# Kernel tuning notes

Hardware: AMD Instinct MI355X
Metric: run time of the kernel (lower is better)

Reference implementation:

```python
import jax, jax.numpy as jnp
import numpy as np

N, E = 50000, 800000          # nodes, edges
F_IN, H, C = 32, 64, 7        # input feats, hidden, classes
EPS = 1e-5                    # BatchNorm eps


def setup_inputs() -> dict:
    key = jax.random.key(0)
    ks = jax.random.split(key, 16)
    inp = {
        "x": jax.random.normal(ks[0], (N, F_IN), jnp.float32),
        "edge_index": jax.random.randint(ks[1], (2, E), 0, N),
        "edge_attr": jax.random.uniform(ks[2], (E, 1), jnp.float32),
    }

    def conv_params(k, cin, cout, i):
        k1, k2 = jax.random.split(k)
        s = 1.0 / np.sqrt(cin)
        inp[f"W{i}"] = jax.random.uniform(k1, (2, cin, cout), jnp.float32, -s, s)  # spline kernel weights
        inp[f"R{i}"] = jax.random.uniform(k2, (cin, cout), jnp.float32, -s, s)     # root weight
        inp[f"B{i}"] = jnp.zeros((cout,), jnp.float32)

    conv_params(ks[3], F_IN, H, 0)
    conv_params(ks[4], H, H, 1)
    conv_params(ks[5], H, C, 2)
    for i in range(2):  # BatchNorm (eval mode: running stats)
        inp[f"G{i}"] = jnp.ones((H,), jnp.float32)
        inp[f"BE{i}"] = jnp.zeros((H,), jnp.float32)
        inp[f"RM{i}"] = 0.1 * jax.random.normal(ks[6 + 2 * i], (H,), jnp.float32)
        inp[f"RV{i}"] = jax.random.uniform(ks[7 + 2 * i], (H,), jnp.float32, 0.5, 1.5)
    return inp


def spline_conv(x, src, dst, u, W, R, B):
    # dim=1, kernel_size=2, degree=1 open B-spline:
    # basis = (1-u, u) with weight indices (0, 1) for u in [0,1).
    basis = jnp.stack([1.0 - u, u], axis=1)               # [E, 2]
    msg = jnp.einsum('ec,ek,kco->eo', x[src], basis, W)    # gather + basis-weighted linear
    agg = jax.ops.segment_sum(msg, dst, num_segments=N)    # scatter-add
    deg = jax.ops.segment_sum(jnp.ones((src.shape[0],), x.dtype), dst, num_segments=N)
    agg = agg / jnp.maximum(deg, 1.0)[:, None]             # aggr='mean' (default)
    return agg + x @ R + B                                 # root weight + bias


def batch_norm(x, g, b, rm, rv):
    return (x - rm) * jax.lax.rsqrt(rv + EPS) * g + b


def reference(x, edge_index, edge_attr,
              W0, R0, B0, W1, R1, B1, W2, R2, B2,
              G0, BE0, RM0, RV0, G1, BE1, RM1, RV1):
    src, dst = edge_index[0], edge_index[1]
    u = edge_attr[:, 0]
    h = spline_conv(x, src, dst, u, W0, R0, B0)
    h = jax.nn.elu(batch_norm(h, G0, BE0, RM0, RV0))
    h = spline_conv(h, src, dst, u, W1, R1, B1)
    h = jax.nn.elu(batch_norm(h, G1, BE1, RM1, RV1))
    h = spline_conv(h, src, dst, u, W2, R2, B2)
    return jax.nn.log_softmax(h, axis=1)
```

## Files before the change

### kernel.cpp

```cpp
#include <hip/hip_runtime.h>
#include <hip/hip_fp16.h>
#include <math.h>

#define NN 50000
#define NE 800000
#define EPSV 1e-5f
#define BSHIFT 7
#define BSIZE 128
#define NB 391
#define CAP 2560

typedef _Float16 h2f   __attribute__((ext_vector_type(2)));
typedef _Float16 f16x8 __attribute__((ext_vector_type(8)));
typedef float    f32x4 __attribute__((ext_vector_type(4)));

__global__ __launch_bounds__(64) void prep_all_kernel(
        const float* __restrict__ W0, const float* __restrict__ R0,
        const float* __restrict__ W1, const float* __restrict__ R1,
        const float* __restrict__ W2, const float* __restrict__ R2,
        __half* __restrict__ Bf0, __half* __restrict__ Bf1, __half* __restrict__ Bf7,
        int* __restrict__ bcursor) {
    int lane = threadIdx.x;
    int bid = blockIdx.x;
    int c = lane & 15;
    int kbase = ((lane >> 4) << 3);
    _Float16 vals[8];
    if (bid < 12) {
        int nt = bid;
        int n = nt * 16 + c;
#pragma unroll
        for (int j = 0; j < 8; ++j) {
            int k = kbase + j;
            float v;
            if (n < 64)       v = W0[k * 64 + n];
            else if (n < 128) v = W0[32 * 64 + k * 64 + (n - 64)];
            else              v = R0[k * 64 + (n - 128)];
            vals[j] = (_Float16)v;
        }
        *reinterpret_cast<f16x8*>(Bf0 + ((size_t)(bid * 64 + lane)) * 8) =
            *reinterpret_cast<f16x8*>(vals);
    } else if (bid < 36) {
        int ksnt = bid - 12;
        int ks = ksnt / 12, nt = ksnt - ks * 12;
        int n = nt * 16 + c;
#pragma unroll
        for (int j = 0; j < 8; ++j) {
            int k = ks * 32 + kbase + j;
            float v;
            if (n < 64)       v = W1[k * 64 + n];
            else if (n < 128) v = W1[64 * 64 + k * 64 + (n - 64)];
            else              v = R1[k * 64 + (n - 128)];
            vals[j] = (_Float16)v;
        }
        *reinterpret_cast<f16x8*>(Bf1 + ((size_t)(ksnt * 64 + lane)) * 8) =
            *reinterpret_cast<f16x8*>(vals);
    } else if (bid < 40) {
        int ksnt = bid - 36;
        int ks = ksnt >> 1, nt = ksnt & 1;
#pragma unroll
        for (int j = 0; j < 8; ++j) {
            int k = ks * 32 + kbase + j;
            float v = 0.f;
            if (nt == 0) {
                if (c < 7)                 v = W2[k * 7 + c];
                else if (c >= 8 && c < 15) v = W2[448 + k * 7 + (c - 8)];
            } else {
                if (c < 7)                 v = R2[k * 7 + c];
            }
            vals[j] = (_Float16)v;
        }
        *reinterpret_cast<f16x8*>(Bf7 + ((size_t)(ksnt * 64 + lane)) * 8) =
            *reinterpret_cast<f16x8*>(vals);
    } else {
        int b = (bid - 40) * 64 + lane;
        if (b < NB) bcursor[b] = b * CAP;
    }
}

template<int CIN, bool AHALF>
__device__ __forceinline__ void gemm_body(int bx, int tid,
                               const void* __restrict__ xin,
                               const __half* __restrict__ Bfrag,
                               const float* __restrict__ Bb,
                               __half2* __restrict__ YabH,
                               float* __restrict__ Z,
                               int n_nodes) {
    const int lane = tid & 63;
    const int wid  = tid >> 6;
    int m0 = (bx * 4 + wid) * 16;
    if (m0 >= n_nodes) return;
    const int KS = CIN / 32;

    f32x4 acc[12];
#pragma unroll
    for (int i = 0; i < 12; ++i) acc[i] = (f32x4){0.f, 0.f, 0.f, 0.f};

    const int arow = m0 + (lane & 15);
    const int koff = ((lane >> 4) << 3);
    const f16x8* bf = reinterpret_cast<const f16x8*>(Bfrag);
#pragma unroll
    for (int ks = 0; ks < KS; ++ks) {
        f16x8 av;
        if constexpr (AHALF) {
            const _Float16* ap = (const _Float16*)xin + (size_t)arow * CIN + ks * 32 + koff;
            av = *reinterpret_cast<const f16x8*>(ap);
        } else {
            const float* ap = (const float*)xin + (size_t)arow * CIN + ks * 32 + koff;
            float4 a0 = *reinterpret_cast<const float4*>(ap);
            float4 a1 = *reinterpret_cast<const float4*>(ap + 4);
            av[0] = (_Float16)a0.x; av[1] = (_Float16)a0.y;
            av[2] = (_Float16)a0.z; av[3] = (_Float16)a0.w;
            av[4] = (_Float16)a1.x; av[5] = (_Float16)a1.y;
            av[6] = (_Float16)a1.z; av[7] = (_Float16)a1.w;
        }
#pragma unroll
        for (int nt = 0; nt < 12; ++nt) {
            f16x8 bv = bf[(ks * 12 + nt) * 64 + lane];
            acc[nt] = __builtin_amdgcn_mfma_f32_16x16x32_f16(av, bv, acc[nt], 0, 0, 0);
        }
    }

    const int c_lo  = lane & 15;
    const int rbase = ((lane >> 4) << 2);
#pragma unroll
    for (int r = 0; r < 4; ++r) {
        int row = m0 + rbase + r;
#pragma unroll
        for (int nt = 0; nt < 4; ++nt) {
            int c = nt * 16 + c_lo;
            YabH[(size_t)row * 64 + c] = __floats2half2_rn(acc[nt][r], acc[nt + 4][r]);
        }
#pragma unroll
        for (int nt = 8; nt < 12; ++nt) {
            int c = (nt - 8) * 16 + c_lo;
            Z[(size_t)row * 64 + c] = acc[nt][r] + Bb[c];
        }
    }
}

__global__ __launch_bounds__(256) void binB_gemm0_kernel(
        const int* __restrict__ src, const int* __restrict__ dst,
        const float* __restrict__ attr, int* __restrict__ bcursor,
        unsigned* __restrict__ es1su, unsigned char* __restrict__ es1dl, int E,
        const float* __restrict__ x, const __half* __restrict__ Bf0,
        const float* __restrict__ Bb0, __half2* __restrict__ YabH,
        float* __restrict__ Z, int n_nodes) {
    __shared__ int hist[NB];
    __shared__ int base[NB];
    if (blockIdx.x >= NB) {
        gemm_body<32, false>(blockIdx.x - NB, threadIdx.x, x, Bf0, Bb0, YabH, Z, n_nodes);
        return;
    }
    for (int i = threadIdx.x; i < NB; i += blockDim.x) hist[i] = 0;
    __syncthreads();
    const int chunk = (E + NB - 1) / NB;
    int e0 = blockIdx.x * chunk;
    int e1 = e0 + chunk; if (e1 > E) e1 = E;
    unsigned su[8]; unsigned char dlv[8]; short bv[8];
#pragma unroll
    for (int j = 0; j < 8; ++j) {
        int e = e0 + threadIdx.x + j * 256;
        if (e < e1) {
            int d = dst[e];
            int b = d >> BSHIFT;
            __half uh = __float2half_rn(attr[e]);
            su[j]  = ((unsigned)src[e] << 16) | (unsigned)__half_as_ushort(uh);
            dlv[j] = (unsigned char)(d & (BSIZE - 1));
            bv[j]  = (short)b;
            atomicAdd(&hist[b], 1);
        }
    }
    __syncthreads();
    for (int i = threadIdx.x; i < NB; i += blockDim.x) {
        int c = hist[i];
        base[i] = c ? atomicAdd(&bcursor[i], c) : 0;
        hist[i] = 0;
    }
    __syncthreads();
#pragma unroll
    for (int j = 0; j < 8; ++j) {
        int e = e0 + threadIdx.x + j * 256;
        if (e < e1) {
            int b = bv[j];
            int slot = base[b] + atomicAdd(&hist[b], 1);
            es1su[slot] = su[j];
            es1dl[slot] = dlv[j];
        }
    }
}

__global__ __launch_bounds__(256) void gemm1_kernel(const __half* __restrict__ h,
                               const __half* __restrict__ Bf1,
                               const float* __restrict__ Bb,
                               __half2* __restrict__ YabH,
                               float* __restrict__ Z, int n_nodes) {
    gemm_body<64, true>(blockIdx.x, threadIdx.x, h, Bf1, Bb, YabH, Z, n_nodes);
}

__global__ __launch_bounds__(256) void placeC_kernel(const int* __restrict__ bcursor,
                                                     const unsigned* __restrict__ es1su,
                                                     const unsigned char* __restrict__ es1dl,
                                                     int2* __restrict__ rowrange,
                                                     uint2* __restrict__ es8) {
    __shared__ int hist[BSIZE];
    __shared__ int stmp[BSIZE];
    __shared__ int cur[BSIZE];
    int b = blockIdx.x;
    int t = threadIdx.x;
    int bs = b * CAP;
    int be = bcursor[b];
    if (t < BSIZE) hist[t] = 0;
    __syncthreads();
    unsigned su[10]; unsigned char dlv[10];
#pragma unroll
    for (int j = 0; j < 10; ++j) {
        int i = bs + t + j * 256;
        if (i < be) {
            su[j]  = es1su[i];
            dlv[j] = es1dl[i];
            atomicAdd(&hist[dlv[j]], 1);
        }
    }
    __syncthreads();
    if (t < BSIZE) {
        int v = hist[t];
        int incl = v;
#pragma unroll
        for (int o = 1; o < 64; o <<= 1) {
            int nv = __shfl_up(incl, o, 64);
            if ((t & 63) >= o) incl += nv;
        }
        stmp[t] = incl;
    }
    __syncthreads();
    if (t < BSIZE) {
        int excl = stmp[t] - hist[t] + ((t >= 64) ? stmp[63] : 0);
        cur[t] = excl;
        int node = b * BSIZE + t;
        if (node < NN) {
            int2 rr; rr.x = bs + excl; rr.y = bs + excl + hist[t];
            rowrange[node] = rr;
        }
    }
    __syncthreads();
#pragma unroll
    for (int j = 0; j < 10; ++j) {
        int i = bs + t + j * 256;
        if (i < be) {
            unsigned r = su[j];
            int dl = dlv[j];
            int slot = bs + atomicAdd(&cur[dl], 1);
            __half uh = __ushort_as_half((unsigned short)(r & 0xffffu));
            __half2 p = __halves2half2(__hsub(__ushort_as_half((unsigned short)0x3C00u), uh), uh);
            uint2 rec;
            rec.x = r >> 16;
            rec.y = *reinterpret_cast<unsigned*>(&p);
            es8[slot] = rec;
        }
    }
}

__global__ __launch_bounds__(256) void gemm7_kernel(const __half* __restrict__ h,
                               const __half* __restrict__ Bf7,
                               const float* __restrict__ Bb,
                               __half* __restrict__ Yab7H,
                               float* __restrict__ Z7,
                               int n_nodes) {
    const int lane = threadIdx.x & 63;
    const int wid  = threadIdx.x >> 6;
    int m0 = (blockIdx.x * 4 + wid) * 16;
    if (m0 >= n_nodes) return;

    f32x4 acc[2];
    acc[0] = (f32x4){0.f, 0.f, 0.f, 0.f};
    acc[1] = (f32x4){0.f, 0.f, 0.f, 0.f};
    const int arow = m0 + (lane & 15);
    const int koff = ((lane >> 4) << 3);
    const f16x8* bf = reinterpret_cast<const f16x8*>(Bf7);
#pragma unroll
    for (int ks = 0; ks < 2; ++ks) {
        f16x8 av = *reinterpret_cast<const f16x8*>(
            (const _Float16*)h + (size_t)arow * 64 + ks * 32 + koff);
#pragma unroll
        for (int nt = 0; nt < 2; ++nt) {
            f16x8 bv = bf[(ks * 2 + nt) * 64 + lane];
            acc[nt] = __builtin_amdgcn_mfma_f32_16x16x32_f16(av, bv, acc[nt], 0, 0, 0);
        }
    }
    const int c_lo  = lane & 15;
    const int rbase = ((lane >> 4) << 2);
#pragma unroll
    for (int r = 0; r < 4; ++r) {
        int row = m0 + rbase + r;
        if (c_lo < 7) {
            Yab7H[(size_t)row * 14 + 2 * c_lo] = __float2half(acc[0][r]);
            Z7[(size_t)row * 7 + c_lo] = acc[1][r] + Bb[c_lo];
        } else if (c_lo >= 8 && c_lo < 15) {
            Yab7H[(size_t)row * 14 + 2 * (c_lo - 8) + 1] = __float2half(acc[0][r]);
        }
    }
}

__global__ void gather64_kernel(const int2* __restrict__ rowrange,
                                const uint2* __restrict__ es8,
                                const __half2* __restrict__ YabH,
                                const float* __restrict__ Z,
                                const float* __restrict__ G, const float* __restrict__ BE,
                                const float* __restrict__ RM, const float* __restrict__ RV,
                                __half* __restrict__ h, int n_nodes) {
    int n = (blockIdx.x * blockDim.x + threadIdx.x) >> 6;
    int lane = threadIdx.x & 63;
    if (n >= n_nodes) return;
    int2 rr = rowrange[n];
    int beg = __builtin_amdgcn_readfirstlane(rr.x);
    int end = __builtin_amdgcn_readfirstlane(rr.y);
    const char* Ybase = (const char*)YabH + 4 * lane;
    float acc0 = 0.f, acc1 = 0.f, acc2 = 0.f, acc3 = 0.f;
    float acc4 = 0.f, acc5 = 0.f, acc6 = 0.f, acc7 = 0.f;
    int i = beg;
    if (i < end && (i & 1)) {
        uint2 q = es8[i];
        __half2 v = *(const __half2*)(Ybase + ((size_t)q.x << 8));
        acc0 = __builtin_amdgcn_fdot2(__builtin_bit_cast(h2f, v), __builtin_bit_cast(h2f, q.y), acc0, false);
        ++i;
    }
    for (; i + 15 < end; i += 16) {
        uint4 q0 = *reinterpret_cast<const uint4*>(es8 + i);
        uint4 q1 = *reinterpret_cast<const uint4*>(es8 + i + 2);
        uint4 q2 = *reinterpret_cast<const uint4*>(es8 + i + 4);
        uint4 q3 = *reinterpret_cast<const uint4*>(es8 + i + 6);
        uint4 q4 = *reinterpret_cast<const uint4*>(es8 + i + 8);
        uint4 q5 = *reinterpret_cast<const uint4*>(es8 + i + 10);
        uint4 q6 = *reinterpret_cast<const uint4*>(es8 + i + 12);
        uint4 q7 = *reinterpret_cast<const uint4*>(es8 + i + 14);
        __half2 v0 = *(const __half2*)(Ybase + ((size_t)q0.x << 8));
        __half2 v1 = *(const __half2*)(Ybase + ((size_t)q0.z << 8));
        __half2 v2 = *(const __half2*)(Ybase + ((size_t)q1.x << 8));
        __half2 v3 = *(const __half2*)(Ybase + ((size_t)q1.z << 8));
        __half2 v4 = *(const __half2*)(Ybase + ((size_t)q2.x << 8));
        __half2 v5 = *(const __half2*)(Ybase + ((size_t)q2.z << 8));
        __half2 v6 = *(const __half2*)(Ybase + ((size_t)q3.x << 8));
        __half2 v7 = *(const __half2*)(Ybase + ((size_t)q3.z << 8));
        __half2 v8 = *(const __half2*)(Ybase + ((size_t)q4.x << 8));
        __half2 v9 = *(const __half2*)(Ybase + ((size_t)q4.z << 8));
        __half2 va = *(const __half2*)(Ybase + ((size_t)q5.x << 8));
        __half2 vb = *(const __half2*)(Ybase + ((size_t)q5.z << 8));
        __half2 vc = *(const __half2*)(Ybase + ((size_t)q6.x << 8));
        __half2 vd = *(const __half2*)(Ybase + ((size_t)q6.z << 8));
        __half2 ve = *(const __half2*)(Ybase + ((size_t)q7.x << 8));
        __half2 vf = *(const __half2*)(Ybase + ((size_t)q7.z << 8));
        acc0 = __builtin_amdgcn_fdot2(__builtin_bit_cast(h2f, v0), __builtin_bit_cast(h2f, q0.y), acc0, false);
        acc1 = __builtin_amdgcn_fdot2(__builtin_bit_cast(h2f, v1), __builtin_bit_cast(h2f, q0.w), acc1, false);
        acc2 = __builtin_amdgcn_fdot2(__builtin_bit_cast(h2f, v2), __builtin_bit_cast(h2f, q1.y), acc2, false);
        acc3 = __builtin_amdgcn_fdot2(__builtin_bit_cast(h2f, v3), __builtin_bit_cast(h2f, q1.w), acc3, false);
        acc4 = __builtin_amdgcn_fdot2(__builtin_bit_cast(h2f, v4), __builtin_bit_cast(h2f, q2.y), acc4, false);
        acc5 = __builtin_amdgcn_fdot2(__builtin_bit_cast(h2f, v5), __builtin_bit_cast(h2f, q2.w), acc5, false);
        acc6 = __builtin_amdgcn_fdot2(__builtin_bit_cast(h2f, v6), __builtin_bit_cast(h2f, q3.y), acc6, false);
        acc7 = __builtin_amdgcn_fdot2(__builtin_bit_cast(h2f, v7), __builtin_bit_cast(h2f, q3.w), acc7, false);
        acc0 = __builtin_amdgcn_fdot2(__builtin_bit_cast(h2f, v8), __builtin_bit_cast(h2f, q4.y), acc0, false);
        acc1 = __builtin_amdgcn_fdot2(__builtin_bit_cast(h2f, v9), __builtin_bit_cast(h2f, q4.w), acc1, false);
        acc2 = __builtin_amdgcn_fdot2(__builtin_bit_cast(h2f, va), __builtin_bit_cast(h2f, q5.y), acc2, false);
        acc3 = __builtin_amdgcn_fdot2(__builtin_bit_cast(h2f, vb), __builtin_bit_cast(h2f, q5.w), acc3, false);
        acc4 = __builtin_amdgcn_fdot2(__builtin_bit_cast(h2f, vc), __builtin_bit_cast(h2f, q6.y), acc4, false);
        acc5 = __builtin_amdgcn_fdot2(__builtin_bit_cast(h2f, vd), __builtin_bit_cast(h2f, q6.w), acc5, false);
        acc6 = __builtin_amdgcn_fdot2(__builtin_bit_cast(h2f, ve), __builtin_bit_cast(h2f, q7.y), acc6, false);
        acc7 = __builtin_amdgcn_fdot2(__builtin_bit_cast(h2f, vf), __builtin_bit_cast(h2f, q7.w), acc7, false);
    }
    for (; i + 7 < end; i += 8) {
        uint4 q0 = *reinterpret_cast<const uint4*>(es8 + i);
        uint4 q1 = *reinterpret_cast<const uint4*>(es8 + i + 2);
        uint4 q2 = *reinterpret_cast<const uint4*>(es8 + i + 4);
        uint4 q3 = *reinterpret_cast<const uint4*>(es8 + i + 6);
        __half2 v0 = *(const __half2*)(Ybase + ((size_t)q0.x << 8));
        __half2 v1 = *(const __half2*)(Ybase + ((size_t)q0.z << 8));
        __half2 v2 = *(const __half2*)(Ybase + ((size_t)q1.x << 8));
        __half2 v3 = *(const __half2*)(Ybase + ((size_t)q1.z << 8));
        __half2 v4 = *(const __half2*)(Ybase + ((size_t)q2.x << 8));
        __half2 v5 = *(const __half2*)(Ybase + ((size_t)q2.z << 8));
        __half2 v6 = *(const __half2*)(Ybase + ((size_t)q3.x << 8));
        __half2 v7 = *(const __half2*)(Ybase + ((size_t)q3.z << 8));
        acc0 = __builtin_amdgcn_fdot2(__builtin_bit_cast(h2f, v0), __builtin_bit_cast(h2f, q0.y), acc0, false);
        acc1 = __builtin_amdgcn_fdot2(__builtin_bit_cast(h2f, v1), __builtin_bit_cast(h2f, q0.w), acc1, false);
        acc2 = __builtin_amdgcn_fdot2(__builtin_bit_cast(h2f, v2), __builtin_bit_cast(h2f, q1.y), acc2, false);
        acc3 = __builtin_amdgcn_fdot2(__builtin_bit_cast(h2f, v3), __builtin_bit_cast(h2f, q1.w), acc3, false);
        acc4 = __builtin_amdgcn_fdot2(__builtin_bit_cast(h2f, v4), __builtin_bit_cast(h2f, q2.y), acc4, false);
        acc5 = __builtin_amdgcn_fdot2(__builtin_bit_cast(h2f, v5), __builtin_bit_cast(h2f, q2.w), acc5, false);
        acc6 = __builtin_amdgcn_fdot2(__builtin_bit_cast(h2f, v6), __builtin_bit_cast(h2f, q3.y), acc6, false);
        acc7 = __builtin_amdgcn_fdot2(__builtin_bit_cast(h2f, v7), __builtin_bit_cast(h2f, q3.w), acc7, false);
    }
    for (; i + 1 < end; i += 2) {
        uint4 q0 = *reinterpret_cast<const uint4*>(es8 + i);
        __half2 v0 = *(const __half2*)(Ybase + ((size_t)q0.x << 8));
        __half2 v1 = *(const __half2*)(Ybase + ((size_t)q0.z << 8));
        acc0 = __builtin_amdgcn_fdot2(__builtin_bit_cast(h2f, v0), __builtin_bit_cast(h2f, q0.y), acc0, false);
        acc1 = __builtin_amdgcn_fdot2(__builtin_bit_cast(h2f, v1), __builtin_bit_cast(h2f, q0.w), acc1, false);
    }
    if (i < end) {
        uint2 q = es8[i];
        __half2 v = *(const __half2*)(Ybase + ((size_t)q.x << 8));
        acc0 = __builtin_amdgcn_fdot2(__builtin_bit_cast(h2f, v), __builtin_bit_cast(h2f, q.y), acc0, false);
    }
    float acc = ((acc0 + acc1) + (acc2 + acc3)) + ((acc4 + acc5) + (acc6 + acc7));
    float degv = (float)(end - beg);
    if (degv < 1.f) degv = 1.f;
    float v = acc / degv + Z[n * 64 + lane];
    v = (v - RM[lane]) * rsqrtf(RV[lane] + EPSV) * G[lane] + BE[lane];
    h[(size_t)n * 64 + lane] = __float2half(v > 0.f ? v : expm1f(v));
}

__global__ void gather7_final_kernel(const int2* __restrict__ rowrange,
                                     const uint2* __restrict__ es8,
                                     const __half2* __restrict__ Yab7H,
                                     const float* __restrict__ Z7,
                                     float* __restrict__ out, int n_nodes) {
    int t = blockIdx.x * blockDim.x + threadIdx.x;
    int n = t >> 3;
    int c = t & 7;
    if (n >= n_nodes) return;
    int2 rr = rowrange[n];
    int beg = rr.x, end = rr.y;
    float acc0 = 0.f, acc1 = 0.f, acc2 = 0.f, acc3 = 0.f;
    if (c < 7) {
        int i = beg;
        for (; i + 3 < end; i += 4) {
            uint2 q0 = es8[i];
            uint2 q1 = es8[i + 1];
            uint2 q2 = es8[i + 2];
            uint2 q3 = es8[i + 3];
            __half2 v0 = Yab7H[(size_t)q0.x * 7 + c];
            __half2 v1 = Yab7H[(size_t)q1.x * 7 + c];
            __half2 v2 = Yab7H[(size_t)q2.x * 7 + c];
            __half2 v3 = Yab7H[(size_t)q3.x * 7 + c];
            acc0 = __builtin_amdgcn_fdot2(__builtin_bit_cast(h2f, v0), __builtin_bit_cast(h2f, q0.y), acc0, false);
            acc1 = __builtin_amdgcn_fdot2(__builtin_bit_cast(h2f, v1), __builtin_bit_cast(h2f, q1.y), acc1, false);
            acc2 = __builtin_amdgcn_fdot2(__builtin_bit_cast(h2f, v2), __builtin_bit_cast(h2f, q2.y), acc2, false);
            acc3 = __builtin_amdgcn_fdot2(__builtin_bit_cast(h2f, v3), __builtin_bit_cast(h2f, q3.y), acc3, false);
        }
        for (; i < end; ++i) {
            uint2 q = es8[i];
            __half2 v = Yab7H[(size_t)q.x * 7 + c];
            acc0 = __builtin_amdgcn_fdot2(__builtin_bit_cast(h2f, v), __builtin_bit_cast(h2f, q.y), acc0, false);
        }
    }
    float acc = (acc0 + acc1) + (acc2 + acc3);
    float degv = (float)(end - beg);
    if (degv < 1.f) degv = 1.f;
    float v = (c < 7) ? (acc / degv + Z7[n * 7 + c]) : -1e30f;
    float m = v;
#pragma unroll
    for (int o = 1; o < 8; o <<= 1) m = fmaxf(m, __shfl_xor(m, o, 8));
    float ex = (c < 7) ? expf(v - m) : 0.f;
    float ssum = ex;
#pragma unroll
    for (int o = 1; o < 8; o <<= 1) ssum += __shfl_xor(ssum, o, 8);
    if (c < 7) out[n * 7 + c] = v - m - logf(ssum);
}

extern "C" void kernel_launch(void* const* d_in, const int* in_sizes, int n_in,
                              void* d_out, int out_size, void* d_ws, size_t ws_size,
                              hipStream_t stream) {
    const float* x    = (const float*)d_in[0];
    const int*   ei   = (const int*)d_in[1];
    const float* attr = (const float*)d_in[2];
    const float* W0 = (const float*)d_in[3];
    const float* R0 = (const float*)d_in[4];
    const float* B0 = (const float*)d_in[5];
    const float* W1 = (const float*)d_in[6];
    const float* R1 = (const float*)d_in[7];
    const float* B1 = (const float*)d_in[8];
    const float* W2 = (const float*)d_in[9];
    const float* R2 = (const float*)d_in[10];
    const float* B2 = (const float*)d_in[11];
    const float* G0  = (const float*)d_in[12];
    const float* BE0 = (const float*)d_in[13];
    const float* RM0 = (const float*)d_in[14];
    const float* RV0 = (const float*)d_in[15];
    const float* G1  = (const float*)d_in[16];
    const float* BE1 = (const float*)d_in[17];
    const float* RM1 = (const float*)d_in[18];
    const float* RV1 = (const float*)d_in[19];

    const int* src = ei;
    const int* dst = ei + NE;
    float* out = (float*)d_out;

    char* ws = (char*)d_ws;
    size_t off = 0;
    auto alloc = [&](size_t bytes) { char* p = ws + off; off += (bytes + 255) & ~size_t(255); return p; };
    int*           bcursor  = (int*)          alloc(NB * sizeof(int));
    int2*          rowrange = (int2*)         alloc((size_t)NN * sizeof(int2));
    unsigned*      es1su    = (unsigned*)     alloc((size_t)NB * CAP * sizeof(unsigned));
    unsigned char* es1dl    = (unsigned char*)alloc((size_t)NB * CAP * sizeof(unsigned char));
    uint2*         es8      = (uint2*)        alloc((size_t)NB * CAP * sizeof(uint2));
    __half*        Bf0      = (__half*)       alloc((size_t)12 * 64 * 8 * sizeof(__half));
    __half*        Bf1      = (__half*)       alloc((size_t)24 * 64 * 8 * sizeof(__half));
    __half*        Bf7      = (__half*)       alloc((size_t)4 * 64 * 8 * sizeof(__half));
    __half2*       YabH     = (__half2*)      alloc((size_t)NN * 64 * sizeof(__half2));
    __half*        Yab7H    = (__half*)       alloc((size_t)NN * 14 * sizeof(__half));
    float*         Z        = (float*)        alloc((size_t)NN * 64 * sizeof(float));
    __half*        h        = (__half*)       alloc((size_t)NN * 64 * sizeof(__half));
    float*         Z7       = (float*)        alloc((size_t)NN * 7 * sizeof(float));

    const int B = 256;
    const int gN64  = (NN * 64 + B - 1) / B;
    const int gN8   = (NN * 8 + B - 1) / B;
    const int gM    = ((NN + 15) / 16 + 3) / 4;
    const int gPrep = 40 + (NB + 63) / 64;

    prep_all_kernel<<<gPrep, 64, 0, stream>>>(W0, R0, W1, R1, W2, R2, Bf0, Bf1, Bf7, bcursor);

    binB_gemm0_kernel<<<NB + gM, B, 0, stream>>>(src, dst, attr, bcursor, es1su, es1dl, NE,
                                                 x, Bf0, B0, YabH, Z, NN);

    placeC_kernel<<<NB, B, 0, stream>>>(bcursor, es1su, es1dl, rowrange, es8);

    gather64_kernel<<<gN64, B, 0, stream>>>(rowrange, es8, YabH, Z, G0, BE0, RM0, RV0, h, NN);

    gemm1_kernel<<<gM, B, 0, stream>>>(h, Bf1, B1, YabH, Z, NN);
    gather64_kernel<<<gN64, B, 0, stream>>>(rowrange, es8, YabH, Z, G1, BE1, RM1, RV1, h, NN);

    gemm7_kernel<<<gM, B, 0, stream>>>(h, Bf7, B2, Yab7H, Z7, NN);
    gather7_final_kernel<<<gN8, B, 0, stream>>>(rowrange, es8, (const __half2*)Yab7H, Z7, out, NN);
}
```

Baseline: 220.0 us.

## Reorder spline conv to aggregate-then-transform and fuse BN/ELU into GEMM epilogue

Layers 0 and 1 now first aggregate basis-weighted neighbor features into a per-node buffer S, then run one MFMA GEMM over [S, x] with a combined weight matrix. Bias and BatchNorm are folded into a precomputed scale/shift applied with ELU in the GEMM epilogue. This shrinks the per-edge gather width (notably for layer 0, which gathers 32-wide inputs instead of 128 transformed halves) and removes the fp32 Z intermediate. In exchange it writes and rereads an extra S buffer and uses more kernel launches.

Measured after the change: 209.3 us. 1.05x faster.

```diff
diff --git a/kernel.cpp b/kernel.cpp
--- a/kernel.cpp
+++ b/kernel.cpp
@@ -18,7 +18,13 @@
         const float* __restrict__ W0, const float* __restrict__ R0,
         const float* __restrict__ W1, const float* __restrict__ R1,
         const float* __restrict__ W2, const float* __restrict__ R2,
+        const float* __restrict__ B0, const float* __restrict__ B1,
+        const float* __restrict__ G0, const float* __restrict__ BE0,
+        const float* __restrict__ RM0, const float* __restrict__ RV0,
+        const float* __restrict__ G1, const float* __restrict__ BE1,
+        const float* __restrict__ RM1, const float* __restrict__ RV1,
         __half* __restrict__ Bf0, __half* __restrict__ Bf1, __half* __restrict__ Bf7,
+        float* __restrict__ bn0, float* __restrict__ bn1,
         int* __restrict__ bcursor) {
     int lane = threadIdx.x;
     int bid = blockIdx.x;
@@ -26,33 +32,29 @@
     int kbase = ((lane >> 4) << 3);
     _Float16 vals[8];
     if (bid < 12) {
-        int nt = bid;
+        int ks = bid >> 2, nt = bid & 3;
         int n = nt * 16 + c;
 #pragma unroll
         for (int j = 0; j < 8; ++j) {
-            int k = kbase + j;
-            float v;
-            if (n < 64)       v = W0[k * 64 + n];
-            else if (n < 128) v = W0[32 * 64 + k * 64 + (n - 64)];
-            else              v = R0[k * 64 + (n - 128)];
+            int kg = ks * 32 + kbase + j;
+            float v = (kg < 64) ? W0[(kg & 1) * 2048 + (kg >> 1) * 64 + n]
+                                : R0[(kg - 64) * 64 + n];
             vals[j] = (_Float16)v;
         }
         *reinterpret_cast<f16x8*>(Bf0 + ((size_t)(bid * 64 + lane)) * 8) =
             *reinterpret_cast<f16x8*>(vals);
     } else if (bid < 36) {
-        int ksnt = bid - 12;
-        int ks = ksnt / 12, nt = ksnt - ks * 12;
+        int t = bid - 12;
+        int ks = t >> 2, nt = t & 3;
         int n = nt * 16 + c;
 #pragma unroll
         for (int j = 0; j < 8; ++j) {
-            int k = ks * 32 + kbase + j;
-            float v;
-            if (n < 64)       v = W1[k * 64 + n];
-            else if (n < 128) v = W1[64 * 64 + k * 64 + (n - 64)];
-            else              v = R1[k * 64 + (n - 128)];
+            int kg = ks * 32 + kbase + j;
+            float v = (kg < 128) ? W1[(kg & 1) * 4096 + (kg >> 1) * 64 + n]
+                                 : R1[(kg - 128) * 64 + n];
             vals[j] = (_Float16)v;
         }
-        *reinterpret_cast<f16x8*>(Bf1 + ((size_t)(ksnt * 64 + lane)) * 8) =
+        *reinterpret_cast<f16x8*>(Bf1 + ((size_t)(t * 64 + lane)) * 8) =
             *reinterpret_cast<f16x8*>(vals);
     } else if (bid < 40) {
         int ksnt = bid - 36;
@@ -71,84 +73,37 @@
         }
         *reinterpret_cast<f16x8*>(Bf7 + ((size_t)(ksnt * 64 + lane)) * 8) =
             *reinterpret_cast<f16x8*>(vals);
+    } else if (bid == 40) {
+        float s = G0[lane] * rsqrtf(RV0[lane] + EPSV);
+        bn0[lane] = s;
+        bn0[64 + lane] = B0[lane] * s + BE0[lane] - RM0[lane] * s;
+    } else if (bid == 41) {
+        float s = G1[lane] * rsqrtf(RV1[lane] + EPSV);
+        bn1[lane] = s;
+        bn1[64 + lane] = B1[lane] * s + BE1[lane] - RM1[lane] * s;
     } else {
-        int b = (bid - 40) * 64 + lane;
+        int b = (bid - 42) * 64 + lane;
         if (b < NB) bcursor[b] = b * CAP;
     }
 }
 
-template<int CIN, bool AHALF>
-__device__ __forceinline__ void gemm_body(int bx, int tid,
-                               const void* __restrict__ xin,
-                               const __half* __restrict__ Bfrag,
-                               const float* __restrict__ Bb,
-                               __half2* __restrict__ YabH,
-                               float* __restrict__ Z,
-                               int n_nodes) {
-    const int lane = tid & 63;
-    const int wid  = tid >> 6;
-    int m0 = (bx * 4 + wid) * 16;
-    if (m0 >= n_nodes) return;
-    const int KS = CIN / 32;
-
-    f32x4 acc[12];
-#pragma unroll
-    for (int i = 0; i < 12; ++i) acc[i] = (f32x4){0.f, 0.f, 0.f, 0.f};
-
-    const int arow = m0 + (lane & 15);
-    const int koff = ((lane >> 4) << 3);
-    const f16x8* bf = reinterpret_cast<const f16x8*>(Bfrag);
-#pragma unroll
-    for (int ks = 0; ks < KS; ++ks) {
-        f16x8 av;
-        if constexpr (AHALF) {
-            const _Float16* ap = (const _Float16*)xin + (size_t)arow * CIN + ks * 32 + koff;
-            av = *reinterpret_cast<const f16x8*>(ap);
-        } else {
-            const float* ap = (const float*)xin + (size_t)arow * CIN + ks * 32 + koff;
-            float4 a0 = *reinterpret_cast<const float4*>(ap);
-            float4 a1 = *reinterpret_cast<const float4*>(ap + 4);
-            av[0] = (_Float16)a0.x; av[1] = (_Float16)a0.y;
-            av[2] = (_Float16)a0.z; av[3] = (_Float16)a0.w;
-            av[4] = (_Float16)a1.x; av[5] = (_Float16)a1.y;
-            av[6] = (_Float16)a1.z; av[7] = (_Float16)a1.w;
-        }
-#pragma unroll
-        for (int nt = 0; nt < 12; ++nt) {
-            f16x8 bv = bf[(ks * 12 + nt) * 64 + lane];
-            acc[nt] = __builtin_amdgcn_mfma_f32_16x16x32_f16(av, bv, acc[nt], 0, 0, 0);
-        }
-    }
-
-    const int c_lo  = lane & 15;
-    const int rbase = ((lane >> 4) << 2);
-#pragma unroll
-    for (int r = 0; r < 4; ++r) {
-        int row = m0 + rbase + r;
-#pragma unroll
-        for (int nt = 0; nt < 4; ++nt) {
-            int c = nt * 16 + c_lo;
-            YabH[(size_t)row * 64 + c] = __floats2half2_rn(acc[nt][r], acc[nt + 4][r]);
-        }
-#pragma unroll
-        for (int nt = 8; nt < 12; ++nt) {
-            int c = (nt - 8) * 16 + c_lo;
-            Z[(size_t)row * 64 + c] = acc[nt][r] + Bb[c];
-        }
-    }
-}
-
-__global__ __launch_bounds__(256) void binB_gemm0_kernel(
+__global__ __launch_bounds__(256) void binB_xh_kernel(
         const int* __restrict__ src, const int* __restrict__ dst,
         const float* __restrict__ attr, int* __restrict__ bcursor,
         unsigned* __restrict__ es1su, unsigned char* __restrict__ es1dl, int E,
-        const float* __restrict__ x, const __half* __restrict__ Bf0,
-        const float* __restrict__ Bb0, __half2* __restrict__ YabH,
-        float* __restrict__ Z, int n_nodes) {
+        const float* __restrict__ x, __half* __restrict__ xh) {
     __shared__ int hist[NB];
     __shared__ int base[NB];
     if (blockIdx.x >= NB) {
-        gemm_body<32, false>(blockIdx.x - NB, threadIdx.x, x, Bf0, Bb0, YabH, Z, n_nodes);
+        int t = (blockIdx.x - NB) * 256 + threadIdx.x;
+        size_t idx = (size_t)t * 8;
+        if (idx < (size_t)NN * 32) {
+            float4 f0 = *reinterpret_cast<const float4*>(x + idx);
+            float4 f1 = *reinterpret_cast<const float4*>(x + idx + 4);
+            _Float16 v[8] = {(_Float16)f0.x, (_Float16)f0.y, (_Float16)f0.z, (_Float16)f0.w,
+                             (_Float16)f1.x, (_Float16)f1.y, (_Float16)f1.z, (_Float16)f1.w};
+            *reinterpret_cast<f16x8*>(xh + idx) = *reinterpret_cast<f16x8*>(v);
+        }
         return;
     }
     for (int i = threadIdx.x; i < NB; i += blockDim.x) hist[i] = 0;
@@ -172,8 +127,8 @@
     }
     __syncthreads();
     for (int i = threadIdx.x; i < NB; i += blockDim.x) {
-        int c = hist[i];
-        base[i] = c ? atomicAdd(&bcursor[i], c) : 0;
+        int cnt = hist[i];
+        base[i] = cnt ? atomicAdd(&bcursor[i], cnt) : 0;
         hist[i] = 0;
     }
     __syncthreads();
@@ -187,14 +142,6 @@
             es1dl[slot] = dlv[j];
         }
     }
-}
-
-__global__ __launch_bounds__(256) void gemm1_kernel(const __half* __restrict__ h,
-                               const __half* __restrict__ Bf1,
-                               const float* __restrict__ Bb,
-                               __half2* __restrict__ YabH,
-                               float* __restrict__ Z, int n_nodes) {
-    gemm_body<64, true>(blockIdx.x, threadIdx.x, h, Bf1, Bb, YabH, Z, n_nodes);
 }
 
 __global__ __launch_bounds__(256) void placeC_kernel(const int* __restrict__ bcursor,
@@ -260,6 +207,217 @@
     }
 }
 
+__global__ __launch_bounds__(256) void gatherS32_kernel(const int2* __restrict__ rowrange,
+                                                        const uint2* __restrict__ es8,
+                                                        const __half* __restrict__ xh,
+                                                        __half* __restrict__ S, int n_nodes) {
+    int n = (blockIdx.x * blockDim.x + threadIdx.x) >> 6;
+    int lane = threadIdx.x & 63;
+    if (n >= n_nodes) return;
+    int2 rr = rowrange[n];
+    int beg = __builtin_amdgcn_readfirstlane(rr.x);
+    int end = __builtin_amdgcn_readfirstlane(rr.y);
+    int c = lane & 31;
+    const __half* xb = xh + c;
+    float a0 = 0.f, a1 = 0.f, a2 = 0.f, a3 = 0.f;
+    float b0 = 0.f, b1 = 0.f, b2 = 0.f, b3 = 0.f;
+    int i = beg + (lane >> 5);
+    for (; i + 6 < end; i += 8) {
+        uint2 q0 = es8[i];
+        uint2 q1 = es8[i + 2];
+        uint2 q2 = es8[i + 4];
+        uint2 q3 = es8[i + 6];
+        float x0 = __half2float(xb[(size_t)q0.x << 5]);
+        float x1 = __half2float(xb[(size_t)q1.x << 5]);
+        float x2 = __half2float(xb[(size_t)q2.x << 5]);
+        float x3 = __half2float(xb[(size_t)q3.x << 5]);
+        __half2 u0 = __builtin_bit_cast(__half2, q0.y);
+        __half2 u1 = __builtin_bit_cast(__half2, q1.y);
+        __half2 u2 = __builtin_bit_cast(__half2, q2.y);
+        __half2 u3 = __builtin_bit_cast(__half2, q3.y);
+        a0 = fmaf(__low2float(u0), x0, a0); b0 = fmaf(__high2float(u0), x0, b0);
+        a1 = fmaf(__low2float(u1), x1, a1); b1 = fmaf(__high2float(u1), x1, b1);
+        a2 = fmaf(__low2float(u2), x2, a2); b2 = fmaf(__high2float(u2), x2, b2);
+        a3 = fmaf(__low2float(u3), x3, a3); b3 = fmaf(__high2float(u3), x3, b3);
+    }
+    for (; i < end; i += 2) {
+        uint2 q = es8[i];
+        float xv = __half2float(xb[(size_t)q.x << 5]);
+        __half2 u = __builtin_bit_cast(__half2, q.y);
+        a0 = fmaf(__low2float(u), xv, a0); b0 = fmaf(__high2float(u), xv, b0);
+    }
+    float a = (a0 + a1) + (a2 + a3);
+    float b = (b0 + b1) + (b2 + b3);
+    a += __shfl_xor(a, 32);
+    b += __shfl_xor(b, 32);
+    float degv = (float)(end - beg);
+    if (degv < 1.f) degv = 1.f;
+    float inv = 1.f / degv;
+    if (lane < 32) {
+        reinterpret_cast<__half2*>(S + (size_t)n * 64)[c] = __floats2half2_rn(a * inv, b * inv);
+    }
+}
+
+__global__ __launch_bounds__(256) void gatherS64_kernel(const int2* __restrict__ rowrange,
+                                                        const uint2* __restrict__ es8,
+                                                        const __half* __restrict__ ht,
+                                                        __half* __restrict__ S, int n_nodes) {
+    int n = (blockIdx.x * blockDim.x + threadIdx.x) >> 6;
+    int lane = threadIdx.x & 63;
+    if (n >= n_nodes) return;
+    int2 rr = rowrange[n];
+    int beg = __builtin_amdgcn_readfirstlane(rr.x);
+    int end = __builtin_amdgcn_readfirstlane(rr.y);
+    const __half* xb = ht + lane;
+    float a0 = 0.f, a1 = 0.f, a2 = 0.f, a3 = 0.f;
+    float b0 = 0.f, b1 = 0.f, b2 = 0.f, b3 = 0.f;
+    int i = beg;
+    if (i < end && (i & 1)) {
+        uint2 q = es8[i];
+        float xv = __half2float(xb[(size_t)q.x << 6]);
+        __half2 u = __builtin_bit_cast(__half2, q.y);
+        a0 = fmaf(__low2float(u), xv, a0); b0 = fmaf(__high2float(u), xv, b0);
+        ++i;
+    }
+    for (; i + 7 < end; i += 8) {
+        uint4 p0 = *reinterpret_cast<const uint4*>(es8 + i);
+        uint4 p1 = *reinterpret_cast<const uint4*>(es8 + i + 2);
+        uint4 p2 = *reinterpret_cast<const uint4*>(es8 + i + 4);
+        uint4 p3 = *reinterpret_cast<const uint4*>(es8 + i + 6);
+        float x0 = __half2float(xb[(size_t)p0.x << 6]);
+        float x1 = __half2float(xb[(size_t)p0.z << 6]);
+        float x2 = __half2float(xb[(size_t)p1.x << 6]);
+        float x3 = __half2float(xb[(size_t)p1.z << 6]);
+        float x4 = __half2float(xb[(size_t)p2.x << 6]);
+        float x5 = __half2float(xb[(size_t)p2.z << 6]);
+        float x6 = __half2float(xb[(size_t)p3.x << 6]);
+        float x7 = __half2float(xb[(size_t)p3.z << 6]);
+        __half2 u0 = __builtin_bit_cast(__half2, p0.y);
+        __half2 u1 = __builtin_bit_cast(__half2, p0.w);
+        __half2 u2 = __builtin_bit_cast(__half2, p1.y);
+        __half2 u3 = __builtin_bit_cast(__half2, p1.w);
+        __half2 u4 = __builtin_bit_cast(__half2, p2.y);
+        __half2 u5 = __builtin_bit_cast(__half2, p2.w);
+        __half2 u6 = __builtin_bit_cast(__half2, p3.y);
+        __half2 u7 = __builtin_bit_cast(__half2, p3.w);
+        a0 = fmaf(__low2float(u0), x0, a0); b0 = fmaf(__high2float(u0), x0, b0);
+        a1 = fmaf(__low2float(u1), x1, a1); b1 = fmaf(__high2float(u1), x1, b1);
+        a2 = fmaf(__low2float(u2), x2, a2); b2 = fmaf(__high2float(u2), x2, b2);
+        a3 = fmaf(__low2float(u3), x3, a3); b3 = fmaf(__high2float(u3), x3, b3);
+        a0 = fmaf(__low2float(u4), x4, a0); b0 = fmaf(__high2float(u4), x4, b0);
+        a1 = fmaf(__low2float(u5), x5, a1); b1 = fmaf(__high2float(u5), x5, b1);
+        a2 = fmaf(__low2float(u6), x6, a2); b2 = fmaf(__high2float(u6), x6, b2);
+        a3 = fmaf(__low2float(u7), x7, a3); b3 = fmaf(__high2float(u7), x7, b3);
+    }
+    for (; i + 1 < end; i += 2) {
+        uint4 p = *reinterpret_cast<const uint4*>(es8 + i);
+        float x0 = __half2float(xb[(size_t)p.x << 6]);
+        float x1 = __half2float(xb[(size_t)p.z << 6]);
+        __half2 u0 = __builtin_bit_cast(__half2, p.y);
+        __half2 u1 = __builtin_bit_cast(__half2, p.w);
+        a0 = fmaf(__low2float(u0), x0, a0); b0 = fmaf(__high2float(u0), x0, b0);
+        a1 = fmaf(__low2float(u1), x1, a1); b1 = fmaf(__high2float(u1), x1, b1);
+    }
+    if (i < end) {
+        uint2 q = es8[i];
+        float xv = __half2float(xb[(size_t)q.x << 6]);
+        __half2 u = __builtin_bit_cast(__half2, q.y);
+        a0 = fmaf(__low2float(u), xv, a0); b0 = fmaf(__high2float(u), xv, b0);
+    }
+    float a = (a0 + a1) + (a2 + a3);
+    float b = (b0 + b1) + (b2 + b3);
+    float degv = (float)(end - beg);
+    if (degv < 1.f) degv = 1.f;
+    float inv = 1.f / degv;
+    reinterpret_cast<__half2*>(S + (size_t)n * 128)[lane] = __floats2half2_rn(a * inv, b * inv);
+}
+
+__global__ __launch_bounds__(256) void gemmL0_kernel(const __half* __restrict__ S,
+                                                     const __half* __restrict__ xh,
+                                                     const __half* __restrict__ Bf0,
+                                                     const float* __restrict__ bn,
+                                                     __half* __restrict__ hout, int n_nodes) {
+    const int lane = threadIdx.x & 63;
+    const int wid  = threadIdx.x >> 6;
+    int m0 = (blockIdx.x * 4 + wid) * 16;
+    if (m0 >= n_nodes) return;
+    f32x4 acc[4];
+#pragma unroll
+    for (int i = 0; i < 4; ++i) acc[i] = (f32x4){0.f, 0.f, 0.f, 0.f};
+    const int arow = m0 + (lane & 15);
+    const int koff = ((lane >> 4) << 3);
+    const f16x8* bf = reinterpret_cast<const f16x8*>(Bf0);
+    const _Float16* sp = (const _Float16*)S  + (size_t)arow * 64 + koff;
+    const _Float16* xp = (const _Float16*)xh + (size_t)arow * 32 + koff;
+    f16x8 a0 = *reinterpret_cast<const f16x8*>(sp);
+    f16x8 a1 = *reinterpret_cast<const f16x8*>(sp + 32);
+    f16x8 a2 = *reinterpret_cast<const f16x8*>(xp);
+#pragma unroll
+    for (int nt = 0; nt < 4; ++nt)
+        acc[nt] = __builtin_amdgcn_mfma_f32_16x16x32_f16(a0, bf[nt * 64 + lane], acc[nt], 0, 0, 0);
+#pragma unroll
+    for (int nt = 0; nt < 4; ++nt)
+        acc[nt] = __builtin_amdgcn_mfma_f32_16x16x32_f16(a1, bf[(4 + nt) * 64 + lane], acc[nt], 0, 0, 0);
+#pragma unroll
+    for (int nt = 0; nt < 4; ++nt)
+        acc[nt] = __builtin_amdgcn_mfma_f32_16x16x32_f16(a2, bf[(8 + nt) * 64 + lane], acc[nt], 0, 0, 0);
+    const int c_lo  = lane & 15;
+    const int rbase = ((lane >> 4) << 2);
+#pragma unroll
+    for (int nt = 0; nt < 4; ++nt) {
+        int cc = nt * 16 + c_lo;
+        float sc = bn[cc], sh = bn[64 + cc];
+#pragma unroll
+        for (int r = 0; r < 4; ++r) {
+            int row = m0 + rbase + r;
+            float v = acc[nt][r] * sc + sh;
+            v = v > 0.f ? v : expm1f(v);
+            hout[(size_t)row * 64 + cc] = __float2half(v);
+        }
+    }
+}
+
+__global__ __launch_bounds__(256) void gemmL1_kernel(const __half* __restrict__ S,
+                                                     const __half* __restrict__ hin,
+                                                     const __half* __restrict__ Bf1,
+                                                     const float* __restrict__ bn,
+                                                     __half* __restrict__ hout, int n_nodes) {
+    const int lane = threadIdx.x & 63;
+    const int wid  = threadIdx.x >> 6;
+    int m0 = (blockIdx.x * 4 + wid) * 16;
+    if (m0 >= n_nodes) return;
+    f32x4 acc[4];
+#pragma unroll
+    for (int i = 0; i < 4; ++i) acc[i] = (f32x4){0.f, 0.f, 0.f, 0.f};
+    const int arow = m0 + (lane & 15);
+    const int koff = ((lane >> 4) << 3);
+    const f16x8* bf = reinterpret_cast<const f16x8*>(Bf1);
+    const _Float16* sp = (const _Float16*)S   + (size_t)arow * 128 + koff;
+    const _Float16* hp = (const _Float16*)hin + (size_t)arow * 64  + koff;
+#pragma unroll
+    for (int ks = 0; ks < 6; ++ks) {
+        f16x8 av = (ks < 4) ? *reinterpret_cast<const f16x8*>(sp + ks * 32)
+                            : *reinterpret_cast<const f16x8*>(hp + (ks - 4) * 32);
+#pragma unroll
+        for (int nt = 0; nt < 4; ++nt)
+            acc[nt] = __builtin_amdgcn_mfma_f32_16x16x32_f16(av, bf[(ks * 4 + nt) * 64 + lane], acc[nt], 0, 0, 0);
+    }
+    const int c_lo  = lane & 15;
+    const int rbase = ((lane >> 4) << 2);
+#pragma unroll
+    for (int nt = 0; nt < 4; ++nt) {
+        int cc = nt * 16 + c_lo;
+        float sc = bn[cc], sh = bn[64 + cc];
+#pragma unroll
+        for (int r = 0; r < 4; ++r) {
+            int row = m0 + rbase + r;
+            float v = acc[nt][r] * sc + sh;
+            v = v > 0.f ? v : expm1f(v);
+            hout[(size_t)row * 64 + cc] = __float2half(v);
+        }
+    }
+}
+
 __global__ __launch_bounds__(256) void gemm7_kernel(const __half* __restrict__ h,
                                const __half* __restrict__ Bf7,
                                const float* __restrict__ Bb,
@@ -299,113 +457,6 @@
             Yab7H[(size_t)row * 14 + 2 * (c_lo - 8) + 1] = __float2half(acc[0][r]);
         }
     }
-}
-
-__global__ void gather64_kernel(const int2* __restrict__ rowrange,
-                                const uint2* __restrict__ es8,
-                                const __half2* __restrict__ YabH,
-                                const float* __restrict__ Z,
-                                const float* __restrict__ G, const float* __restrict__ BE,
-                                const float* __restrict__ RM, const float* __restrict__ RV,
-                                __half* __restrict__ h, int n_nodes) {
-    int n = (blockIdx.x * blockDim.x + threadIdx.x) >> 6;
-    int lane = threadIdx.x & 63;
-    if (n >= n_nodes) return;
-    int2 rr = rowrange[n];
-    int beg = __builtin_amdgcn_readfirstlane(rr.x);
-    int end = __builtin_amdgcn_readfirstlane(rr.y);
-    const char* Ybase = (const char*)YabH + 4 * lane;
-    float acc0 = 0.f, acc1 = 0.f, acc2 = 0.f, acc3 = 0.f;
-    float acc4 = 0.f, acc5 = 0.f, acc6 = 0.f, acc7 = 0.f;
-    int i = beg;
-    if (i < end && (i & 1)) {
-        uint2 q = es8[i];
-        __half2 v = *(const __half2*)(Ybase + ((size_t)q.x << 8));
-        acc0 = __builtin_amdgcn_fdot2(__builtin_bit_cast(h2f, v), __builtin_bit_cast(h2f, q.y), acc0, false);
-        ++i;
-    }
-    for (; i + 15 < end; i += 16) {
-        uint4 q0 = *reinterpret_cast<const uint4*>(es8 + i);
-        uint4 q1 = *reinterpret_cast<const uint4*>(es8 + i + 2);
-        uint4 q2 = *reinterpret_cast<const uint4*>(es8 + i + 4);
-        uint4 q3 = *reinterpret_cast<const uint4*>(es8 + i + 6);
-        uint4 q4 = *reinterpret_cast<const uint4*>(es8 + i + 8);
-        uint4 q5 = *reinterpret_cast<const uint4*>(es8 + i + 10);
-        uint4 q6 = *reinterpret_cast<const uint4*>(es8 + i + 12);
-        uint4 q7 = *reinterpret_cast<const uint4*>(es8 + i + 14);
-        __half2 v0 = *(const __half2*)(Ybase + ((size_t)q0.x << 8));
-        __half2 v1 = *(const __half2*)(Ybase + ((size_t)q0.z << 8));
-        __half2 v2 = *(const __half2*)(Ybase + ((size_t)q1.x << 8));
-        __half2 v3 = *(const __half2*)(Ybase + ((size_t)q1.z << 8));
-        __half2 v4 = *(const __half2*)(Ybase + ((size_t)q2.x << 8));
-        __half2 v5 = *(const __half2*)(Ybase + ((size_t)q2.z << 8));
-        __half2 v6 = *(const __half2*)(Ybase + ((size_t)q3.x << 8));
-        __half2 v7 = *(const __half2*)(Ybase + ((size_t)q3.z << 8));
-        __half2 v8 = *(const __half2*)(Ybase + ((size_t)q4.x << 8));
-        __half2 v9 = *(const __half2*)(Ybase + ((size_t)q4.z << 8));
-        __half2 va = *(const __half2*)(Ybase + ((size_t)q5.x << 8));
-        __half2 vb = *(const __half2*)(Ybase + ((size_t)q5.z << 8));
-        __half2 vc = *(const __half2*)(Ybase + ((size_t)q6.x << 8));
-        __half2 vd = *(const __half2*)(Ybase + ((size_t)q6.z << 8));
-        __half2 ve = *(const __half2*)(Ybase + ((size_t)q7.x << 8));
-        __half2 vf = *(const __half2*)(Ybase + ((size_t)q7.z << 8));
-        acc0 = __builtin_amdgcn_fdot2(__builtin_bit_cast(h2f, v0), __builtin_bit_cast(h2f, q0.y), acc0, false);
-        acc1 = __builtin_amdgcn_fdot2(__builtin_bit_cast(h2f, v1), __builtin_bit_cast(h2f, q0.w), acc1, false);
-        acc2 = __builtin_amdgcn_fdot2(__builtin_bit_cast(h2f, v2), __builtin_bit_cast(h2f, q1.y), acc2, false);
-        acc3 = __builtin_amdgcn_fdot2(__builtin_bit_cast(h2f, v3), __builtin_bit_cast(h2f, q1.w), acc3, false);
-        acc4 = __builtin_amdgcn_fdot2(__builtin_bit_cast(h2f, v4), __builtin_bit_cast(h2f, q2.y), acc4, false);
-        acc5 = __builtin_amdgcn_fdot2(__builtin_bit_cast(h2f, v5), __builtin_bit_cast(h2f, q2.w), acc5, false);
-        acc6 = __builtin_amdgcn_fdot2(__builtin_bit_cast(h2f, v6), __builtin_bit_cast(h2f, q3.y), acc6, false);
-        acc7 = __builtin_amdgcn_fdot2(__builtin_bit_cast(h2f, v7), __builtin_bit_cast(h2f, q3.w), acc7, false);
-        acc0 = __builtin_amdgcn_fdot2(__builtin_bit_cast(h2f, v8), __builtin_bit_cast(h2f, q4.y), acc0, false);
-        acc1 = __builtin_amdgcn_fdot2(__builtin_bit_cast(h2f, v9), __builtin_bit_cast(h2f, q4.w), acc1, false);
-        acc2 = __builtin_amdgcn_fdot2(__builtin_bit_cast(h2f, va), __builtin_bit_cast(h2f, q5.y), acc2, false);
-        acc3 = __builtin_amdgcn_fdot2(__builtin_bit_cast(h2f, vb), __builtin_bit_cast(h2f, q5.w), acc3, false);
-        acc4 = __builtin_amdgcn_fdot2(__builtin_bit_cast(h2f, vc), __builtin_bit_cast(h2f, q6.y), acc4, false);
-        acc5 = __builtin_amdgcn_fdot2(__builtin_bit_cast(h2f, vd), __builtin_bit_cast(h2f, q6.w), acc5, false);
-        acc6 = __builtin_amdgcn_fdot2(__builtin_bit_cast(h2f, ve), __builtin_bit_cast(h2f, q7.y), acc6, false);
-        acc7 = __builtin_amdgcn_fdot2(__builtin_bit_cast(h2f, vf), __builtin_bit_cast(h2f, q7.w), acc7, false);
-    }
-    for (; i + 7 < end; i += 8) {
-        uint4 q0 = *reinterpret_cast<const uint4*>(es8 + i);
-        uint4 q1 = *reinterpret_cast<const uint4*>(es8 + i + 2);
-        uint4 q2 = *reinterpret_cast<const uint4*>(es8 + i + 4);
-        uint4 q3 = *reinterpret_cast<const uint4*>(es8 + i + 6);
-        __half2 v0 = *(const __half2*)(Ybase + ((size_t)q0.x << 8));
-        __half2 v1 = *(const __half2*)(Ybase + ((size_t)q0.z << 8));
-        __half2 v2 = *(const __half2*)(Ybase + ((size_t)q1.x << 8));
-        __half2 v3 = *(const __half2*)(Ybase + ((size_t)q1.z << 8));
-        __half2 v4 = *(const __half2*)(Ybase + ((size_t)q2.x << 8));
-        __half2 v5 = *(const __half2*)(Ybase + ((size_t)q2.z << 8));
-        __half2 v6 = *(const __half2*)(Ybase + ((size_t)q3.x << 8));
-        __half2 v7 = *(const __half2*)(Ybase + ((size_t)q3.z << 8));
-        acc0 = __builtin_amdgcn_fdot2(__builtin_bit_cast(h2f, v0), __builtin_bit_cast(h2f, q0.y), acc0, false);
-        acc1 = __builtin_amdgcn_fdot2(__builtin_bit_cast(h2f, v1), __builtin_bit_cast(h2f, q0.w), acc1, false);
-        acc2 = __builtin_amdgcn_fdot2(__builtin_bit_cast(h2f, v2), __builtin_bit_cast(h2f, q1.y), acc2, false);
-        acc3 = __builtin_amdgcn_fdot2(__builtin_bit_cast(h2f, v3), __builtin_bit_cast(h2f, q1.w), acc3, false);
-        acc4 = __builtin_amdgcn_fdot2(__builtin_bit_cast(h2f, v4), __builtin_bit_cast(h2f, q2.y), acc4, false);
-        acc5 = __builtin_amdgcn_fdot2(__builtin_bit_cast(h2f, v5), __builtin_bit_cast(h2f, q2.w), acc5, false);
-        acc6 = __builtin_amdgcn_fdot2(__builtin_bit_cast(h2f, v6), __builtin_bit_cast(h2f, q3.y), acc6, false);
-        acc7 = __builtin_amdgcn_fdot2(__builtin_bit_cast(h2f, v7), __builtin_bit_cast(h2f, q3.w), acc7, false);
-    }
-    for (; i + 1 < end; i += 2) {
-        uint4 q0 = *reinterpret_cast<const uint4*>(es8 + i);
-        __half2 v0 = *(const __half2*)(Ybase + ((size_t)q0.x << 8));
-        __half2 v1 = *(const __half2*)(Ybase + ((size_t)q0.z << 8));
-        acc0 = __builtin_amdgcn_fdot2(__builtin_bit_cast(h2f, v0), __builtin_bit_cast(h2f, q0.y), acc0, false);
-        acc1 = __builtin_amdgcn_fdot2(__builtin_bit_cast(h2f, v1), __builtin_bit_cast(h2f, q0.w), acc1, false);
-    }
-    if (i < end) {
-        uint2 q = es8[i];
-        __half2 v = *(const __half2*)(Ybase + ((size_t)q.x << 8));
-        acc0 = __builtin_amdgcn_fdot2(__builtin_bit_cast(h2f, v), __builtin_bit_cast(h2f, q.y), acc0, false);
-    }
-    float acc = ((acc0 + acc1) + (acc2 + acc3)) + ((acc4 + acc5) + (acc6 + acc7));
-    float degv = (float)(end - beg);
-    if (degv < 1.f) degv = 1.f;
-    float v = acc / degv + Z[n * 64 + lane];
-    v = (v - RM[lane]) * rsqrtf(RV[lane] + EPSV) * G[lane] + BE[lane];
-    h[(size_t)n * 64 + lane] = __float2half(v > 0.f ? v : expm1f(v));
 }
 
 __global__ void gather7_final_kernel(const int2* __restrict__ rowrange,
@@ -495,30 +546,36 @@
     __half*        Bf0      = (__half*)       alloc((size_t)12 * 64 * 8 * sizeof(__half));
     __half*        Bf1      = (__half*)       alloc((size_t)24 * 64 * 8 * sizeof(__half));
     __half*        Bf7      = (__half*)       alloc((size_t)4 * 64 * 8 * sizeof(__half));
-    __half2*       YabH     = (__half2*)      alloc((size_t)NN * 64 * sizeof(__half2));
+    float*         bn0      = (float*)        alloc(128 * sizeof(float));
+    float*         bn1      = (float*)        alloc(128 * sizeof(float));
+    __half*        xh       = (__half*)       alloc((size_t)NN * 32 * sizeof(__half));
+    __half*        S        = (__half*)       alloc((size_t)NN * 128 * sizeof(__half));
+    __half*        h0       = (__half*)       alloc((size_t)NN * 64 * sizeof(__half));
+    __half*        h1       = (__half*)       alloc((size_t)NN * 64 * sizeof(__half));
     __half*        Yab7H    = (__half*)       alloc((size_t)NN * 14 * sizeof(__half));
-    float*         Z        = (float*)        alloc((size_t)NN * 64 * sizeof(float));
-    __half*        h        = (__half*)       alloc((size_t)NN * 64 * sizeof(__half));
     float*         Z7       = (float*)        alloc((size_t)NN * 7 * sizeof(float));
 
     const int B = 256;
-    const int gN64  = (NN * 64 + B - 1) / B;
+    const int gM    = ((NN + 15) / 16 + 3) / 4;
+    const int gGath = (NN * 64) / (B);
     const int gN8   = (NN * 8 + B - 1) / B;
-    const int gM    = ((NN + 15) / 16 + 3) / 4;
-    const int gPrep = 40 + (NB + 63) / 64;
-
-    prep_all_kernel<<<gPrep, 64, 0, stream>>>(W0, R0, W1, R1, W2, R2, Bf0, Bf1, Bf7, bcursor);
-
-    binB_gemm0_kernel<<<NB + gM, B, 0, stream>>>(src, dst, attr, bcursor, es1su, es1dl, NE,
-                                                 x, Bf0, B0, YabH, Z, NN);
+    const int gConv = ((NN * 32 / 8) + B - 1) / B;
+    const int gPrep = 42 + (NB + 63) / 64;
+
+    prep_all_kernel<<<gPrep, 64, 0, stream>>>(W0, R0, W1, R1, W2, R2, B0, B1,
+                                              G0, BE0, RM0, RV0, G1, BE1, RM1, RV1,
+                                              Bf0, Bf1, Bf7, bn0, bn1, bcursor);
+
+    binB_xh_kernel<<<NB + gConv, B, 0, stream>>>(src, dst, attr, bcursor, es1su, es1dl, NE, x, xh);
 
     placeC_kernel<<<NB, B, 0, stream>>>(bcursor, es1su, es1dl, rowrange, es8);
 
-    gather64_kernel<<<gN64, B, 0, stream>>>(rowrange, es8, YabH, Z, G0, BE0, RM0, RV0, h, NN);
-
-    gemm1_kernel<<<gM, B, 0, stream>>>(h, Bf1, B1, YabH, Z, NN);
-    gather64_kernel<<<gN64, B, 0, stream>>>(rowrange, es8, YabH, Z, G1, BE1, RM1, RV1, h, NN);
-
-    gemm7_kernel<<<gM, B, 0, stream>>>(h, Bf7, B2, Yab7H, Z7, NN);
+    gatherS32_kernel<<<gGath, B, 0, stream>>>(rowrange, es8, xh, S, NN);
+    gemmL0_kernel<<<gM, B, 0, stream>>>(S, xh, Bf0, bn0, h0, NN);
+
+    gatherS64_kernel<<<gGath, B, 0, stream>>>(rowrange, es8, h0, S, NN);
+    gemmL1_kernel<<<gM, B, 0, stream>>>(S, h0, Bf1, bn1, h1, NN);
+
+    gemm7_kernel<<<gM, B, 0, stream>>>(h1, Bf7, B2, Yab7H, Z7, NN);
     gather7_final_kernel<<<gN8, B, 0, stream>>>(rowrange, es8, (const __half2*)Yab7H, Z7, out, NN);
 }
```
